# Optimization experiments

Hardware: AMD Instinct MI355X
Metric: run time of the kernel (lower is better)

The kernel has to match this reference:

```python
import jax, jax.numpy as jnp
import numpy as np
from jax.scipy.linalg import solve_triangular

REG = 1e-6  # reg_covar added to covariance diagonal
LOG2PI = float(np.log(2.0 * np.pi))
RESP_EPS = 10.0 * float(np.finfo(np.float32).eps)


def _log_gauss(X, means, covs):
    # X: [N,D], means: [K,D], covs: [K,D,D] -> per-sample per-component log N(x|mu_k, Sigma_k): [N,K]
    K, D = means.shape
    eye = jnp.eye(D, dtype=X.dtype)
    chol = jnp.linalg.cholesky(covs + REG * eye)                      # [K,D,D]
    diff = X[None, :, :] - means[:, None, :]                          # [K,N,D]
    sol = jax.vmap(lambda L, d: solve_triangular(L, d.T, lower=True))(chol, diff)  # [K,D,N]
    maha = jnp.sum(sol * sol, axis=1)                                 # [K,N]
    logdet = jnp.sum(jnp.log(jnp.diagonal(chol, axis1=1, axis2=2)), axis=1)  # [K] = 0.5*log|Sigma|
    return (-0.5 * (D * LOG2PI + maha) - logdet[:, None]).T           # [N,K]


def _em_step(X, weights, means, covs):
    N, D = X.shape
    # E-step: responsibilities via stable logsumexp
    lp = _log_gauss(X, means, covs) + jnp.log(weights)[None, :]       # [N,K]
    log_norm = jax.scipy.special.logsumexp(lp, axis=1)                # [N]
    resp = jnp.exp(lp - log_norm[:, None])                            # [N,K]
    # M-step (MLE)
    nk = resp.sum(axis=0) + RESP_EPS                                  # [K]
    new_w = nk / N
    new_means = (resp.T @ X) / nk[:, None]                            # [K,D]
    diff = X[None, :, :] - new_means[:, None, :]                      # [K,N,D]
    new_covs = jnp.einsum('kn,knd,kne->kde', resp.T, diff, diff) / nk[:, None, None]
    new_covs = new_covs + REG * jnp.eye(D, dtype=X.dtype)
    return new_w, new_means, new_covs


def reference(X, weights, means, covariances, n_iter):
    # Normalize provided weights (uniform init in the torch module)
    w0 = weights / jnp.sum(weights)

    def step(carry, _):
        w, m, c = carry
        return _em_step(X, w, m, c), None

    (w, m, c), _ = jax.lax.scan(step, (w0, means, covariances), xs=None, length=n_iter)
    # Final per-sample log-likelihood under the fitted mixture (lower bound)
    lp = _log_gauss(X, m, c) + jnp.log(w)[None, :]
    return jax.scipy.special.logsumexp(lp, axis=1)                    # [N]


def setup_inputs() -> dict:
    key = jax.random.key(0)
    kx, km = jax.random.split(key)
    N, D, K = 100000, 32, 16
    X = jax.random.normal(kx, (N, D), dtype=jnp.float32)
    weights = jnp.ones((K,), dtype=jnp.float32) / K
    means = jax.random.normal(km, (K, D), dtype=jnp.float32)
    covariances = jnp.tile(jnp.eye(D, dtype=jnp.float32)[None], (K, 1, 1))
    return {"X": X, "weights": weights, "means": means, "covariances": covariances, "n_iter": 5}
```

## Files before the change

### kernel.cpp

```cpp
#include <hip/hip_runtime.h>
#include <math.h>

#define REGC 1e-6f
#define LOG2PI 1.83787706640934534f
#define RESP_EPS 1.1920929e-6f

#define PART_K 561
#define RS 16

typedef __attribute__((ext_vector_type(8))) short short8;
typedef __attribute__((ext_vector_type(4))) float f32x4;
typedef unsigned short ushort_t;
typedef unsigned int uint_t;

#define STC(p, v) __hip_atomic_store((p), (v), __ATOMIC_RELAXED, __HIP_MEMORY_SCOPE_AGENT)
#define LDC(p)    __hip_atomic_load((p), __ATOMIC_RELAXED, __HIP_MEMORY_SCOPE_AGENT)

__device__ __forceinline__ ushort_t f2bf(float x) {
    uint_t u = __float_as_uint(x);
    uint_t r = (u + 0x7fffu + ((u >> 16) & 1u)) >> 16;
    return (ushort_t)r;
}
__device__ __forceinline__ float bf2f(ushort_t h) {
    return __uint_as_float(((uint_t)h) << 16);
}
__device__ __forceinline__ f32x4 shx4(f32x4 v, int m) {
    f32x4 r;
#pragma unroll
    for (int i = 0; i < 4; ++i) r[i] = __shfl_xor(v[i], m);
    return r;
}
__device__ __forceinline__ f32x4 sel4(bool s, f32x4 b, f32x4 a) {
    f32x4 r;
#pragma unroll
    for (int i = 0; i < 4; ++i) r[i] = s ? b[i] : a[i];
    return r;
}
__device__ __forceinline__ short8 pack_rx(const float* r8, const short8 bh, float& row) {
    uint_t u[8];
#pragma unroll
    for (int jj = 0; jj < 8; ++jj) {
        float av = r8[jj] * bf2f((ushort_t)bh[jj]);
        row += av;
        u[jj] = __float_as_uint(av) + 0x8000u;
    }
    short8 out;
    uint_t* o = (uint_t*)&out;
    o[0] = __builtin_amdgcn_perm(u[1], u[0], 0x07060302);
    o[1] = __builtin_amdgcn_perm(u[3], u[2], 0x07060302);
    o[2] = __builtin_amdgcn_perm(u[5], u[4], 0x07060302);
    o[3] = __builtin_amdgcn_perm(u[7], u[6], 0x07060302);
    return out;
}

__global__ __launch_bounds__(256) void gmm_prep(const float* __restrict__ X,
                                                const float* __restrict__ w,
                                                const float* __restrict__ mu,
                                                const float* __restrict__ cov,
                                                ushort_t* __restrict__ Xh,
                                                ushort_t* __restrict__ Xl,
                                                ushort_t* __restrict__ XTH,
                                                ushort_t* __restrict__ Wh,
                                                ushort_t* __restrict__ Wl,
                                                float* __restrict__ Bv,
                                                float* __restrict__ Cc,
                                                int* __restrict__ cnt,
                                                int N, int NCB) {
    int t = threadIdx.x;
    if ((int)blockIdx.x < NCB) {
        int chunk = blockIdx.x;
        __shared__ float xsh[32][33];
        int s = t >> 3, q = t & 7;
        int n = chunk * 32 + s;
        float4 v = make_float4(0.f, 0.f, 0.f, 0.f);
        if (n < N) v = ((const float4*)(X + (size_t)n * 32))[q];
        float vv[4] = { v.x, v.y, v.z, v.w };
        xsh[s][q * 4 + 0] = v.x; xsh[s][q * 4 + 1] = v.y;
        xsh[s][q * 4 + 2] = v.z; xsh[s][q * 4 + 3] = v.w;
        if (n < N) {
            ushort_t h[4], l[4];
#pragma unroll
            for (int i = 0; i < 4; ++i) {
                h[i] = f2bf(vv[i]);
                l[i] = f2bf(vv[i] - bf2f(h[i]));
            }
            size_t o = (size_t)n * 32 + q * 4;
            *(uint2*)(Xh + o) = make_uint2((uint_t)h[0] | ((uint_t)h[1] << 16),
                                           (uint_t)h[2] | ((uint_t)h[3] << 16));
            *(uint2*)(Xl + o) = make_uint2((uint_t)l[0] | ((uint_t)l[1] << 16),
                                           (uint_t)l[2] | ((uint_t)l[3] << 16));
        }
        __syncthreads();
        int di = t >> 7;
        int lane = (t >> 1) & 63;
        int jj0 = (t & 1) * 4;
        int c = lane & 15, quad = lane >> 4;
        int d = di * 16 + c;
        ushort_t fh[4];
#pragma unroll
        for (int i = 0; i < 4; ++i) fh[i] = f2bf(xsh[quad * 8 + jj0 + i][d]);
        size_t fo = ((size_t)(chunk * 2 + di) * 64 + lane) * 8 + jj0;
        *(uint2*)(XTH + fo) = make_uint2((uint_t)fh[0] | ((uint_t)fh[1] << 16),
                                         (uint_t)fh[2] | ((uint_t)fh[3] << 16));
        return;
    }
    int k = (int)blockIdx.x - NCB;
    __shared__ float L[32][33];
    __shared__ float Ai[32][33];
    if (t >= 64) {
        if (k == 0 && t - 64 < 8) cnt[t - 64] = 0;
        return;
    }
    const float* cv = cov + (size_t)k * 1024;
    const float* muk = mu + (size_t)k * 32;
#pragma unroll
    for (int rep = 0; rep < 16; ++rep) {
        int idx = rep * 64 + t;
        int i = idx >> 5, j = idx & 31;
        L[i][j] = cv[idx] + (i == j ? REGC : 0.f);
    }
    asm volatile("" ::: "memory");
#pragma unroll
    for (int j = 0; j < 32; ++j) {
        float s = L[j][j];
#pragma unroll
        for (int p = 0; p < j; ++p) { float v = L[j][p]; s -= v * v; }
        float dj = sqrtf(s);
        if (t > j && t < 32) {
            float s2 = L[t][j];
#pragma unroll
            for (int p = 0; p < j; ++p) s2 -= L[t][p] * L[j][p];
            L[t][j] = s2 / dj;
        }
        if (t == j) L[j][j] = dj;
        asm volatile("" ::: "memory");
    }
    if (t < 32) {
        float ai[32];
#pragma unroll
        for (int r = 0; r < 32; ++r) {
            float s = (r == t) ? 1.f : 0.f;
#pragma unroll
            for (int p = 0; p < r; ++p) s -= L[r][p] * ai[p];
            ai[r] = s / L[r][r];
        }
#pragma unroll
        for (int r = 0; r < 32; ++r) Ai[r][t] = ai[r];
    }
    asm volatile("" ::: "memory");
#pragma unroll
    for (int rep = 0; rep < 16; ++rep) {
        int idx = rep * 64 + t;
        int i = idx >> 5, j = idx & 31;
        float v = Ai[i][j];
        ushort_t h = f2bf(v);
        Wh[(size_t)(k * 32 + i) * 32 + j] = h;
        Wl[(size_t)(k * 32 + i) * 32 + j] = f2bf(v - bf2f(h));
    }
    if (t < 32) {
        float s = 0.f;
#pragma unroll
        for (int j = 0; j < 32; ++j) s += Ai[t][j] * muk[j];
        Bv[k * 32 + t] = s;
    }
    float wsum = 0.f;
#pragma unroll
    for (int i = 0; i < 16; ++i) wsum += w[i];
    float lv = (t < 32) ? logf(L[t & 31][t & 31]) : 0.f;
#pragma unroll
    for (int off = 1; off < 32; off <<= 1) lv += __shfl_xor(lv, off);
    if (t == 0) Cc[k] = logf(w[k] / wsum) - 0.5f * 32.0f * LOG2PI - lv;
}

__global__ __launch_bounds__(512)
void gmm_emstep(const ushort_t* __restrict__ Xh, const ushort_t* __restrict__ Xl,
                const ushort_t* __restrict__ XTH,
                const ushort_t* __restrict__ Wh, const ushort_t* __restrict__ Wl,
                const float* __restrict__ Bv, const float* __restrict__ Cc,
                float* __restrict__ part, int N) {
    __shared__ float rsh[16][260];
    int t = threadIdx.x;
    int wave = t >> 6, lane = t & 63;
    int quad = lane >> 4, c = lane & 15;
    int bid = (int)blockIdx.x;

    int wstart0 = bid * 256 + wave * 32;
    bool dup = (wstart0 + 32 > N);
    int wst = dup ? ((N >= 32) ? N - 32 : 0) : wstart0;

    size_t xo0 = (size_t)(wst + c) * 32 + quad * 8;
    size_t xo1 = (size_t)(wst + 16 + c) * 32 + quad * 8;
    short8 ah0 = *(const short8*)(Xh + xo0);
    short8 al0 = *(const short8*)(Xl + xo0);
    short8 ah1 = *(const short8*)(Xh + xo1);
    short8 al1 = *(const short8*)(Xl + xo1);

    short8 xt0[8], xt1[8];
#pragma unroll
    for (int ch = 0; ch < 8; ++ch) {
        size_t fb = (((size_t)(bid * 8 + ch)) * 128 + lane) * 8;
        xt0[ch] = *(const short8*)(XTH + fb);
        xt1[ch] = *(const short8*)(XTH + fb + 512);
    }

    {
        f32x4 p0[2], p1[2], p2[2], p3[2], fin[2];
        size_t wb0 = (size_t)c * 32 + quad * 8;
        short8 nbh0 = *(const short8*)(Wh + wb0);
        short8 nbl0 = *(const short8*)(Wl + wb0);
        short8 nbh1 = *(const short8*)(Wh + wb0 + 512);
        short8 nbl1 = *(const short8*)(Wl + wb0 + 512);
#pragma unroll
        for (int k = 0; k < 16; ++k) {
            short8 bh0 = nbh0, bl0 = nbl0, bh1 = nbh1, bl1 = nbl1;
            if (k < 15) {
                size_t wn = (size_t)((k + 1) * 32 + c) * 32 + quad * 8;
                nbh0 = *(const short8*)(Wh + wn);
                nbl0 = *(const short8*)(Wl + wn);
                nbh1 = *(const short8*)(Wh + wn + 512);
                nbl1 = *(const short8*)(Wl + wn + 512);
            }
            float bv0 = Bv[k * 32 + c];
            float bv1 = Bv[k * 32 + 16 + c];
#pragma unroll
            for (int tt = 0; tt < 2; ++tt) {
                short8 ah = tt ? ah1 : ah0;
                short8 al = tt ? al1 : al0;
                f32x4 a0 = {0.f, 0.f, 0.f, 0.f};
                f32x4 a1 = {0.f, 0.f, 0.f, 0.f};
                a0 = __builtin_amdgcn_mfma_f32_16x16x32_bf16(ah, bh0, a0, 0, 0, 0);
                a0 = __builtin_amdgcn_mfma_f32_16x16x32_bf16(ah, bl0, a0, 0, 0, 0);
                a0 = __builtin_amdgcn_mfma_f32_16x16x32_bf16(al, bh0, a0, 0, 0, 0);
                a1 = __builtin_amdgcn_mfma_f32_16x16x32_bf16(ah, bh1, a1, 0, 0, 0);
                a1 = __builtin_amdgcn_mfma_f32_16x16x32_bf16(ah, bl1, a1, 0, 0, 0);
                a1 = __builtin_amdgcn_mfma_f32_16x16x32_bf16(al, bh1, a1, 0, 0, 0);
                f32x4 ms;
#pragma unroll
                for (int r = 0; r < 4; ++r) {
                    float d0 = a0[r] - bv0;
                    float d1 = a1[r] - bv1;
                    ms[r] = fmaf(d0, d0, d1 * d1);
                }
                if ((k & 1) == 0) { p0[tt] = ms; }
                else {
                    f32x4 a = p0[tt] + shx4(p0[tt], 1);
                    f32x4 b = ms + shx4(ms, 1);
                    f32x4 v = sel4((c & 1) != 0, b, a);
                    if ((k & 2) == 0) { p1[tt] = v; }
                    else {
                        a = p1[tt] + shx4(p1[tt], 2); b = v + shx4(v, 2); v = sel4((c & 2) != 0, b, a);
                        if ((k & 4) == 0) { p2[tt] = v; }
                        else {
                            a = p2[tt] + shx4(p2[tt], 4); b = v + shx4(v, 4); v = sel4((c & 4) != 0, b, a);
                            if ((k & 8) == 0) { p3[tt] = v; }
                            else {
                                a = p3[tt] + shx4(p3[tt], 8); b = v + shx4(v, 8);
                                fin[tt] = sel4((c & 8) != 0, b, a);
                            }
                        }
                    }
                }
            }
        }
        float ccv = Cc[c];
#pragma unroll
        for (int tt = 0; tt < 2; ++tt) {
            f32x4 lp;
#pragma unroll
            for (int r = 0; r < 4; ++r) lp[r] = ccv - 0.5f * fin[tt][r];
            f32x4 mx = lp;
#pragma unroll
            for (int off = 1; off < 16; off <<= 1) {
                f32x4 s = shx4(mx, off);
#pragma unroll
                for (int r = 0; r < 4; ++r) mx[r] = fmaxf(mx[r], s[r]);
            }
            f32x4 e;
#pragma unroll
            for (int r = 0; r < 4; ++r) e[r] = __expf(lp[r] - mx[r]);
            f32x4 sm = e;
#pragma unroll
            for (int off = 1; off < 16; off <<= 1) sm = sm + shx4(sm, off);
            f32x4 sv;
#pragma unroll
            for (int r = 0; r < 4; ++r) sv[r] = dup ? 0.f : e[r] / sm[r];
            *(f32x4*)&rsh[c][wave * 32 + tt * 16 + quad * 4] = sv;
        }
    }
    __syncthreads();

    {
        f32x4 q00[2], q01[2], q11[2];
#pragma unroll
        for (int kk = 0; kk < 2; ++kk) {
            q00[kk] = (f32x4){0.f, 0.f, 0.f, 0.f};
            q01[kk] = (f32x4){0.f, 0.f, 0.f, 0.f};
            q11[kk] = (f32x4){0.f, 0.f, 0.f, 0.f};
        }
        float row0[2] = {0.f, 0.f}, row1[2] = {0.f, 0.f}, corner[2] = {0.f, 0.f};

#pragma unroll
        for (int ch = 0; ch < 8; ++ch) {
            short8 bh0 = xt0[ch];
            short8 bh1 = xt1[ch];
#pragma unroll
            for (int kk = 0; kk < 2; ++kk) {
                int k = wave + kk * 8;
                float r8[8];
#pragma unroll
                for (int jj = 0; jj < 8; ++jj) r8[jj] = rsh[k][ch * 32 + quad * 8 + jj];
                corner[kk] += ((r8[0] + r8[1]) + (r8[2] + r8[3])) +
                              ((r8[4] + r8[5]) + (r8[6] + r8[7]));
                short8 a0 = pack_rx(r8, bh0, row0[kk]);
                short8 a1 = pack_rx(r8, bh1, row1[kk]);
                q00[kk] = __builtin_amdgcn_mfma_f32_16x16x32_bf16(a0, bh0, q00[kk], 0, 0, 0);
                q01[kk] = __builtin_amdgcn_mfma_f32_16x16x32_bf16(a0, bh1, q01[kk], 0, 0, 0);
                q11[kk] = __builtin_amdgcn_mfma_f32_16x16x32_bf16(a1, bh1, q11[kk], 0, 0, 0);
            }
        }
#pragma unroll
        for (int kk = 0; kk < 2; ++kk) {
            row0[kk] += __shfl_xor(row0[kk], 16);  row0[kk] += __shfl_xor(row0[kk], 32);
            row1[kk] += __shfl_xor(row1[kk], 16);  row1[kk] += __shfl_xor(row1[kk], 32);
            corner[kk] += __shfl_xor(corner[kk], 16);  corner[kk] += __shfl_xor(corner[kk], 32);

            int k = wave + kk * 8;
            float* pb = part + ((size_t)bid * 16 + k) * PART_K;
#pragma unroll
            for (int r = 0; r < 4; ++r) {
                int i = quad * 4 + r;
                int base = i * 32 - ((i * (i + 1)) >> 1);
                if (c >= i) pb[base + c] = q00[kk][r];
                pb[base + 16 + c] = q01[kk][r];
                int i2 = 16 + i;
                if (c >= i) pb[i2 * 32 - ((i2 * (i2 + 1)) >> 1) + 16 + c] = q11[kk][r];
            }
            if (quad == 0) {
                pb[528 + c] = row0[kk];
                pb[528 + 16 + c] = row1[kk];
            }
            if (lane == 0) pb[560] = corner[kk];
        }
    }
}

__global__ __launch_bounds__(256) void gmm_redsolve(const float* __restrict__ part,
                                                    float* __restrict__ part2,
                                                    int* __restrict__ cnt,
                                                    ushort_t* __restrict__ Wh,
                                                    ushort_t* __restrict__ Wl,
                                                    float* __restrict__ Bv,
                                                    float* __restrict__ Cc,
                                                    int N, int MB, int it) {
    int bid = (int)blockIdx.x;
    int t = threadIdx.x;
    int k = bid & 15, g = bid >> 4;
    int nb = (MB + RS - 1) / RS;
    int b0 = g * nb;
    int b1 = b0 + nb; if (b1 > MB) b1 = MB;

    for (int idx = t; idx < PART_K; idx += 256) {
        float s = 0.f;
#pragma unroll 4
        for (int b = b0; b < b1; ++b)
            s += part[((size_t)b * 16 + k) * PART_K + idx];
        STC(&part2[((size_t)g * 16 + k) * PART_K + idx], s);
    }
    __syncthreads();
    if (t == 0)
        __hip_atomic_fetch_add(&cnt[it], 1, __ATOMIC_RELEASE, __HIP_MEMORY_SCOPE_AGENT);
    if (g != 0) return;

    if (t == 0) {
        while (__hip_atomic_load(&cnt[it], __ATOMIC_ACQUIRE, __HIP_MEMORY_SCOPE_AGENT) < 256)
            __builtin_amdgcn_s_sleep(4);
    }
    __syncthreads();

    __shared__ float Ssh[561];
    __shared__ float Lsh[1056];
    __shared__ float Aish[1056];
    __shared__ float meansh[32];

    for (int idx = t; idx < PART_K; idx += 256) {
        float s = 0.f;
#pragma unroll
        for (int b = 0; b < RS; ++b)
            s += LDC(&part2[((size_t)b * 16 + k) * PART_K + idx]);
        Ssh[idx] = s;
    }
    __syncthreads();
    float nk = Ssh[560] + RESP_EPS;
    float inv = 1.f / nk;
    if (t < 32) meansh[t] = Ssh[528 + t] * inv;
    __syncthreads();
#pragma unroll
    for (int i0 = 0; i0 < 4; ++i0) {
        int i = i0 * 8 + (t >> 5), j = t & 31;
        int a = i < j ? i : j;
        int b2 = i < j ? j : i;
        float cv = Ssh[a * 32 - ((a * (a + 1)) >> 1) + b2];
        Lsh[i * 33 + j] = cv * inv - meansh[i] * meansh[j] + ((i == j) ? 2.f * REGC : 0.f);
    }
    __syncthreads();
    if (t < 64) {
#pragma unroll
        for (int j = 0; j < 32; ++j) {
            float s = Lsh[j * 33 + j];
#pragma unroll
            for (int p = 0; p < j; ++p) { float v = Lsh[j * 33 + p]; s -= v * v; }
            float dj = sqrtf(s);
            if (t > j && t < 32) {
                float s2 = Lsh[t * 33 + j];
#pragma unroll
                for (int p = 0; p < j; ++p) s2 -= Lsh[t * 33 + p] * Lsh[j * 33 + p];
                Lsh[t * 33 + j] = s2 / dj;
            }
            if (t == j) Lsh[j * 33 + j] = dj;
            asm volatile("" ::: "memory");
        }
        if (t < 32) {
            float ai[32];
#pragma unroll
            for (int r = 0; r < 32; ++r) {
                float s = (r == t) ? 1.f : 0.f;
#pragma unroll
                for (int p = 0; p < r; ++p) s -= Lsh[r * 33 + p] * ai[p];
                ai[r] = s / Lsh[r * 33 + r];
            }
#pragma unroll
            for (int r = 0; r < 32; ++r) Aish[r * 33 + t] = ai[r];
        }
    }
    __syncthreads();
#pragma unroll
    for (int i0 = 0; i0 < 4; ++i0) {
        int i = i0 * 8 + (t >> 5), j = t & 31;
        float v = Aish[i * 33 + j];
        ushort_t h = f2bf(v);
        Wh[(size_t)(k * 32 + i) * 32 + j] = h;
        Wl[(size_t)(k * 32 + i) * 32 + j] = f2bf(v - bf2f(h));
    }
    if (t < 32) {
        float s = 0.f;
#pragma unroll
        for (int j = 0; j < 32; ++j) s += Aish[t * 33 + j] * meansh[j];
        Bv[k * 32 + t] = s;
    }
    float lv = (t < 32) ? logf(Lsh[(t & 31) * 33 + (t & 31)]) : 0.f;
#pragma unroll
    for (int off = 1; off < 32; off <<= 1) lv += __shfl_xor(lv, off);
    if (t == 0) Cc[k] = logf(nk / (float)N) - 0.5f * 32.0f * LOG2PI - lv;
}

__global__ __launch_bounds__(256, 2) void gmm_estep_fin(const ushort_t* __restrict__ Xh,
                                                        const ushort_t* __restrict__ Xl,
                                                        const ushort_t* __restrict__ Wh,
                                                        const ushort_t* __restrict__ Wl,
                                                        const float* __restrict__ Bv,
                                                        const float* __restrict__ Cc,
                                                        float* __restrict__ out,
                                                        int N) {
    int t = threadIdx.x;
    int wave = t >> 6, lane = t & 63;
    int quad = lane >> 4, c = lane & 15;
    int wstart = (blockIdx.x * 4 + wave) * 32;
    if (wstart + 32 > N) wstart = (N >= 32) ? (N - 32) : 0;
    bool al4 = ((N & 3) == 0);

    size_t xo0 = (size_t)(wstart + c) * 32 + quad * 8;
    size_t xo1 = (size_t)(wstart + 16 + c) * 32 + quad * 8;
    short8 ah0 = *(const short8*)(Xh + xo0);
    short8 al0 = *(const short8*)(Xl + xo0);
    short8 ah1 = *(const short8*)(Xh + xo1);
    short8 al1 = *(const short8*)(Xl + xo1);

    f32x4 p0[2], p1[2], p2[2], p3[2], fin[2];
#pragma unroll
    for (int k = 0; k < 16; ++k) {
        size_t w0 = (size_t)(k * 32 + c) * 32 + quad * 8;
        size_t w1 = w0 + 512;
        short8 bh0 = *(const short8*)(Wh + w0);
        short8 bl0 = *(const short8*)(Wl + w0);
        short8 bh1 = *(const short8*)(Wh + w1);
        short8 bl1 = *(const short8*)(Wl + w1);
        float bv0 = Bv[k * 32 + c];
        float bv1 = Bv[k * 32 + 16 + c];
#pragma unroll
        for (int tt = 0; tt < 2; ++tt) {
            short8 ah = tt ? ah1 : ah0;
            short8 al = tt ? al1 : al0;
            f32x4 a0 = {0.f, 0.f, 0.f, 0.f};
            f32x4 a1 = {0.f, 0.f, 0.f, 0.f};
            a0 = __builtin_amdgcn_mfma_f32_16x16x32_bf16(ah, bh0, a0, 0, 0, 0);
            a0 = __builtin_amdgcn_mfma_f32_16x16x32_bf16(ah, bl0, a0, 0, 0, 0);
            a0 = __builtin_amdgcn_mfma_f32_16x16x32_bf16(al, bh0, a0, 0, 0, 0);
            a1 = __builtin_amdgcn_mfma_f32_16x16x32_bf16(ah, bh1, a1, 0, 0, 0);
            a1 = __builtin_amdgcn_mfma_f32_16x16x32_bf16(ah, bl1, a1, 0, 0, 0);
            a1 = __builtin_amdgcn_mfma_f32_16x16x32_bf16(al, bh1, a1, 0, 0, 0);
            f32x4 ms;
#pragma unroll
            for (int r = 0; r < 4; ++r) {
                float d0 = a0[r] - bv0;
                float d1 = a1[r] - bv1;
                ms[r] = fmaf(d0, d0, d1 * d1);
            }
            if ((k & 1) == 0) { p0[tt] = ms; }
            else {
                f32x4 a = p0[tt] + shx4(p0[tt], 1);
                f32x4 b = ms + shx4(ms, 1);
                f32x4 v = sel4((c & 1) != 0, b, a);
                if ((k & 2) == 0) { p1[tt] = v; }
                else {
                    a = p1[tt] + shx4(p1[tt], 2); b = v + shx4(v, 2); v = sel4((c & 2) != 0, b, a);
                    if ((k & 4) == 0) { p2[tt] = v; }
                    else {
                        a = p2[tt] + shx4(p2[tt], 4); b = v + shx4(v, 4); v = sel4((c & 4) != 0, b, a);
                        if ((k & 8) == 0) { p3[tt] = v; }
                        else {
                            a = p3[tt] + shx4(p3[tt], 8); b = v + shx4(v, 8);
                            fin[tt] = sel4((c & 8) != 0, b, a);
                        }
                    }
                }
            }
        }
    }
    float ccv = Cc[c];
#pragma unroll
    for (int tt = 0; tt < 2; ++tt) {
        f32x4 lp;
#pragma unroll
        for (int r = 0; r < 4; ++r) lp[r] = ccv - 0.5f * fin[tt][r];
        f32x4 mx = lp;
#pragma unroll
        for (int off = 1; off < 16; off <<= 1) {
            f32x4 s = shx4(mx, off);
#pragma unroll
            for (int r = 0; r < 4; ++r) mx[r] = fmaxf(mx[r], s[r]);
        }
        f32x4 e;
#pragma unroll
        for (int r = 0; r < 4; ++r) e[r] = __expf(lp[r] - mx[r]);
        f32x4 sm = e;
#pragma unroll
        for (int off = 1; off < 16; off <<= 1) sm = sm + shx4(sm, off);
        if (c == 0) {
            int nb = wstart + tt * 16 + quad * 4;
            f32x4 o;
#pragma unroll
            for (int r = 0; r < 4; ++r) o[r] = mx[r] + __logf(sm[r]);
            if (al4) *(f32x4*)(out + nb) = o;
            else { for (int r = 0; r < 4; ++r) out[nb + r] = o[r]; }
        }
    }
}

extern "C" void kernel_launch(void* const* d_in, const int* in_sizes, int n_in,
                              void* d_out, int out_size, void* d_ws, size_t ws_size,
                              hipStream_t stream) {
    const float* X   = (const float*)d_in[0];
    const float* w   = (const float*)d_in[1];
    const float* mu  = (const float*)d_in[2];
    const float* cov = (const float*)d_in[3];
    const int NITER = 5;
    int N = in_sizes[0] / 32;
    int MB = (N + 255) / 256;
    int NCB = MB * 8;

    float* ws = (float*)d_ws;
    float*    Bv = ws;
    float*    Cc = ws + 512;
    ushort_t* Wh = (ushort_t*)(ws + 528);
    ushort_t* Wl = (ushort_t*)(ws + 8720);
    ushort_t* Xh = (ushort_t*)(ws + 16912);
    ushort_t* Xl = (ushort_t*)(ws + 16912 + (size_t)16 * N);
    size_t xt0 = 16912 + (size_t)32 * N;
    size_t XTHf = (size_t)NCB * 512;
    ushort_t* XTH = (ushort_t*)(ws + xt0);
    float*  part2 = ws + xt0 + XTHf;
    float*  part  = part2 + (size_t)RS * 16 * PART_K;
    int*    cnt   = (int*)(part + (size_t)MB * 16 * PART_K);

    float* out = (float*)d_out;

    int eblocks = ((N + 31) / 32 + 3) / 4;

    gmm_prep<<<NCB + 16, 256, 0, stream>>>(X, w, mu, cov, Xh, Xl, XTH, Wh, Wl,
                                           Bv, Cc, cnt, N, NCB);

    for (int it = 0; it < NITER; ++it) {
        gmm_emstep<<<MB, 512, 0, stream>>>(Xh, Xl, XTH, Wh, Wl, Bv, Cc, part, N);
        gmm_redsolve<<<256, 256, 0, stream>>>(part, part2, cnt, Wh, Wl, Bv, Cc,
                                              N, MB, it);
    }
    gmm_estep_fin<<<eblocks, 256, 0, stream>>>(Xh, Xl, Wh, Wl, Bv, Cc, out, N);
}
```

Before: 455.5 us.

## Restructure partial-sum reduction into contiguous row ranges binned in shared memory

The first reduction stage now has each of 128 blocks read a contiguous range of partial-sum rows (covering all components). Loads are software-pipelined and accumulated into per-component bins in shared memory. Previously 256 blocks each strided over one component's rows. The second stage sums 128 partials per component instead of 16, and the shared bin array is reused for the solve buffers. This targets coalescing and streaming of the part array, at the cost of a longer final serial sum and a large shared-memory footprint per block.

```diff
diff --git a/kernel.cpp b/kernel.cpp
--- a/kernel.cpp
+++ b/kernel.cpp
@@ -6,7 +6,7 @@
 #define RESP_EPS 1.1920929e-6f
 
 #define PART_K 561
-#define RS 16
+#define R1B 128
 
 typedef __attribute__((ext_vector_type(8))) short short8;
 typedef __attribute__((ext_vector_type(4))) float f32x4;
@@ -354,40 +354,67 @@
                                                     int N, int MB, int it) {
     int bid = (int)blockIdx.x;
     int t = threadIdx.x;
-    int k = bid & 15, g = bid >> 4;
-    int nb = (MB + RS - 1) / RS;
-    int b0 = g * nb;
-    int b1 = b0 + nb; if (b1 > MB) b1 = MB;
-
-    for (int idx = t; idx < PART_K; idx += 256) {
-        float s = 0.f;
-#pragma unroll 4
-        for (int b = b0; b < b1; ++b)
-            s += part[((size_t)b * 16 + k) * PART_K + idx];
-        STC(&part2[((size_t)g * 16 + k) * PART_K + idx], s);
+    __shared__ float BIN[16 * 561];
+
+    for (int i = t; i < 16 * 561; i += 256) BIN[i] = 0.f;
+    __syncthreads();
+
+    int rows = MB * 16;
+    int rpb = (rows + R1B - 1) / R1B;
+    int r0 = bid * rpb;
+    int r1 = r0 + rpb; if (r1 > rows) r1 = rows;
+
+    {
+        float c0 = 0.f, c1 = 0.f, c2 = 0.f;
+        if (r0 < r1) {
+            const float* sp = part + (size_t)r0 * PART_K;
+            c0 = sp[t]; c1 = sp[t + 256]; if (t < 49) c2 = sp[t + 512];
+        }
+        for (int r = r0; r < r1; ++r) {
+            float n0 = 0.f, n1 = 0.f, n2 = 0.f;
+            if (r + 1 < r1) {
+                const float* sp = part + (size_t)(r + 1) * PART_K;
+                n0 = sp[t]; n1 = sp[t + 256]; if (t < 49) n2 = sp[t + 512];
+            }
+            float* dst = BIN + (r & 15) * 561;
+            dst[t] += c0; dst[t + 256] += c1; if (t < 49) dst[t + 512] += c2;
+            c0 = n0; c1 = n1; c2 = n2;
+        }
+    }
+    __syncthreads();
+
+    for (int i = t; i < 16 * 561; i += 256) {
+        int ki = i / 561, idx = i - ki * 561;
+        STC(&part2[((size_t)ki * R1B + bid) * 561 + idx], BIN[i]);
     }
     __syncthreads();
     if (t == 0)
         __hip_atomic_fetch_add(&cnt[it], 1, __ATOMIC_RELEASE, __HIP_MEMORY_SCOPE_AGENT);
-    if (g != 0) return;
+    if (bid >= 16) return;
 
     if (t == 0) {
-        while (__hip_atomic_load(&cnt[it], __ATOMIC_ACQUIRE, __HIP_MEMORY_SCOPE_AGENT) < 256)
+        while (__hip_atomic_load(&cnt[it], __ATOMIC_ACQUIRE, __HIP_MEMORY_SCOPE_AGENT) < R1B)
             __builtin_amdgcn_s_sleep(4);
     }
     __syncthreads();
 
-    __shared__ float Ssh[561];
-    __shared__ float Lsh[1056];
-    __shared__ float Aish[1056];
-    __shared__ float meansh[32];
-
-    for (int idx = t; idx < PART_K; idx += 256) {
-        float s = 0.f;
-#pragma unroll
-        for (int b = 0; b < RS; ++b)
-            s += LDC(&part2[((size_t)b * 16 + k) * PART_K + idx]);
-        Ssh[idx] = s;
+    int k = bid;
+    float* Ssh   = BIN;
+    float* Lsh   = BIN + 576;
+    float* Aish  = Lsh + 1056;
+    float* meansh = Aish + 1056;
+
+    {
+        const float* s2 = part2 + (size_t)k * R1B * 561;
+        float a0 = 0.f, a1 = 0.f, a2 = 0.f;
+#pragma unroll 4
+        for (int g = 0; g < R1B; ++g) {
+            const float* sp = s2 + (size_t)g * 561;
+            a0 += LDC(sp + t);
+            a1 += LDC(sp + t + 256);
+            if (t < 49) a2 += LDC(sp + t + 512);
+        }
+        Ssh[t] = a0; Ssh[t + 256] = a1; if (t < 49) Ssh[t + 512] = a2;
     }
     __syncthreads();
     float nk = Ssh[560] + RESP_EPS;
@@ -579,7 +606,7 @@
     size_t XTHf = (size_t)NCB * 512;
     ushort_t* XTH = (ushort_t*)(ws + xt0);
     float*  part2 = ws + xt0 + XTHf;
-    float*  part  = part2 + (size_t)RS * 16 * PART_K;
+    float*  part  = part2 + (size_t)16 * R1B * 561;
     int*    cnt   = (int*)(part + (size_t)MB * 16 * PART_K);
 
     float* out = (float*)d_out;
@@ -591,7 +618,7 @@
 
     for (int it = 0; it < NITER; ++it) {
         gmm_emstep<<<MB, 512, 0, stream>>>(Xh, Xl, XTH, Wh, Wl, Bv, Cc, part, N);
-        gmm_redsolve<<<256, 256, 0, stream>>>(part, part2, cnt, Wh, Wl, Bv, Cc,
+        gmm_redsolve<<<R1B, 256, 0, stream>>>(part, part2, cnt, Wh, Wl, Bv, Cc,
                                               N, MB, it);
     }
     gmm_estep_fin<<<eblocks, 256, 0, stream>>>(Xh, Xl, Wh, Wl, Bv, Cc, out, N);
```

Result: slower. 682.3 us (+49.8%).
